# Performance work log

Hardware: AMD Instinct MI355X
Metric: run time of the kernel (lower is better)

## Reference

```python
import jax, jax.numpy as jnp
import numpy as np

N_HEADS = 6

def setup_inputs() -> dict:
    key = jax.random.key(0)
    k1, k2, k3 = jax.random.split(key, 3)
    B, T, C = 256, 256, 192
    x = jax.random.normal(k1, (B, T, C), dtype=jnp.float32)
    w_qkv = jax.random.normal(k2, (3 * C, C), dtype=jnp.float32) * (1.0 / np.sqrt(C))
    w_out = jax.random.normal(k3, (C, C), dtype=jnp.float32) * (1.0 / np.sqrt(C))
    return {"x": x, "w_qkv": w_qkv, "w_out": w_out}

def reference(x, w_qkv, w_out):
    B, T, C = x.shape
    H = N_HEADS
    D = C // H  # head_dim = 32
    qkv = (x @ w_qkv.T).reshape(B, T, 3, H, D)
    q, k, v = qkv[:, :, 0], qkv[:, :, 1], qkv[:, :, 2]  # [B,T,H,D]
    scale = 1.0 / jnp.sqrt(jnp.asarray(D, dtype=x.dtype))
    scores = jnp.einsum('bqhd,bkhd->bhqk', q, k) * scale  # [B,H,T,T]
    causal = jnp.tril(jnp.ones((T, T), dtype=bool))
    scores = jnp.where(causal[None, None], scores, jnp.finfo(x.dtype).min)
    attn = jax.nn.softmax(scores, axis=-1)
    y = jnp.einsum('bhqk,bkhd->bqhd', attn, v).reshape(B, T, C)
    return y @ w_out.T
```

## Files before the change

### kernel.cpp

```cpp
#include <hip/hip_runtime.h>


using f32x4  = __attribute__((ext_vector_type(4))) float;
using bf16x8 = __attribute__((ext_vector_type(8))) __bf16;
using u16x8  = __attribute__((ext_vector_type(8))) unsigned short;
using i32x4  = __attribute__((ext_vector_type(4))) int;

constexpr int Bn = 256;
constexpr int Tn = 256;
constexpr int Cn = 192;
constexpr int Hn = 6;
constexpr int Dn = 32;
constexpr int Mn = Bn * Tn;
constexpr float QSCALE = 0.2550533f;

__device__ __forceinline__ unsigned short f2bf(float f) {
  unsigned int u = __builtin_bit_cast(unsigned int, f);
  u += 0x7fffu + ((u >> 16) & 1u);
  return (unsigned short)(u >> 16);
}

__device__ __forceinline__ unsigned int cvtpk(float lo, float hi) {
  unsigned int r;
  asm("v_cvt_pk_bf16_f32 %0, %1, %2" : "=v"(r) : "v"(lo), "v"(hi));
  return r;
}

__device__ __forceinline__ f32x4 mfma16x16x32(u16x8 a, u16x8 b, f32x4 c) {
  return __builtin_amdgcn_mfma_f32_16x16x32_bf16(
      __builtin_bit_cast(bf16x8, a), __builtin_bit_cast(bf16x8, b), c, 0, 0, 0);
}

__global__ __launch_bounds__(256) void k_qkv(const float* __restrict__ x,
                                             const float* __restrict__ wqkv,
                                             unsigned short* __restrict__ qg,
                                             unsigned short* __restrict__ kg,
                                             unsigned short* __restrict__ vg) {
  __shared__ unsigned short As[64][200];
  __shared__ unsigned short Bs[64][200];
  const int m0 = blockIdx.x * 64;
  const int n0 = blockIdx.y * 64;
  const int tid = threadIdx.x;

#pragma unroll
  for (int it = 0; it < 12; ++it) {
    int f = tid + it * 256;
    int row = f / 48, c4 = (f % 48) * 4;
    float4 va = *reinterpret_cast<const float4*>(&x[(size_t)(m0 + row) * Cn + c4]);
    ushort4 ua; ua.x = f2bf(va.x); ua.y = f2bf(va.y); ua.z = f2bf(va.z); ua.w = f2bf(va.w);
    *reinterpret_cast<ushort4*>(&As[row][c4]) = ua;
    float4 vb = *reinterpret_cast<const float4*>(&wqkv[(size_t)(n0 + row) * Cn + c4]);
    ushort4 ub; ub.x = f2bf(vb.x); ub.y = f2bf(vb.y); ub.z = f2bf(vb.z); ub.w = f2bf(vb.w);
    *reinterpret_cast<ushort4*>(&Bs[row][c4]) = ub;
  }
  __syncthreads();

  const int wv = tid >> 6, lane = tid & 63, llo = lane & 15, lhi = lane >> 4;
  const int wm = (wv >> 1) * 32, wn = (wv & 1) * 32;
  f32x4 acc[2][2] = {};
#pragma unroll
  for (int ks = 0; ks < 6; ++ks) {
    u16x8 a[2], b[2];
#pragma unroll
    for (int i = 0; i < 2; ++i)
      a[i] = *reinterpret_cast<const u16x8*>(&As[wm + 16 * i + llo][ks * 32 + lhi * 8]);
#pragma unroll
    for (int j = 0; j < 2; ++j)
      b[j] = *reinterpret_cast<const u16x8*>(&Bs[wn + 16 * j + llo][ks * 32 + lhi * 8]);
#pragma unroll
    for (int i = 0; i < 2; ++i)
#pragma unroll
      for (int j = 0; j < 2; ++j)
        acc[i][j] = mfma16x16x32(a[i], b[j], acc[i][j]);
  }
#pragma unroll
  for (int i = 0; i < 2; ++i)
#pragma unroll
    for (int j = 0; j < 2; ++j)
#pragma unroll
      for (int r = 0; r < 4; ++r) {
        int mg = m0 + wm + 16 * i + lhi * 4 + r;
        int ng = n0 + wn + 16 * j + llo;
        int s = ng / 192;
        int rem = ng - s * 192;
        int h = rem >> 5, d = rem & 31;
        int bb = mg >> 8, t = mg & 255;
        float val = acc[i][j][r];
        unsigned short* dst = (s == 0) ? qg : (s == 1) ? kg : vg;
        float sv = (s == 0) ? val * QSCALE : val;
        dst[((size_t)(bb * Hn + h) * Tn + t) * Dn + d] = f2bf(sv);
      }
}

__global__ __launch_bounds__(256, 3) void k_attn(const unsigned short* __restrict__ qg,
                                                 const unsigned short* __restrict__ kg,
                                                 const unsigned short* __restrict__ vg,
                                                 unsigned short* __restrict__ yg) {
  __shared__ unsigned short Ks[256][40];
  __shared__ unsigned short Vt[32][264];
  const int bh = blockIdx.x;
  const int b = bh / Hn, h = bh - b * Hn;
  const size_t base = (size_t)bh * Tn * Dn;
  const int tid = threadIdx.x;

  {
    int row = tid;
    const unsigned short* kp = kg + base + (size_t)row * Dn;
    *reinterpret_cast<uint4*>(&Ks[row][0])  = *reinterpret_cast<const uint4*>(kp + 0);
    *reinterpret_cast<uint4*>(&Ks[row][8])  = *reinterpret_cast<const uint4*>(kp + 8);
    *reinterpret_cast<uint4*>(&Ks[row][16]) = *reinterpret_cast<const uint4*>(kp + 16);
    *reinterpret_cast<uint4*>(&Ks[row][24]) = *reinterpret_cast<const uint4*>(kp + 24);
    const unsigned short* vp = vg + base + (size_t)row * Dn;
    u16x8 v0 = *reinterpret_cast<const u16x8*>(vp + 0);
    u16x8 v1 = *reinterpret_cast<const u16x8*>(vp + 8);
    u16x8 v2 = *reinterpret_cast<const u16x8*>(vp + 16);
    u16x8 v3 = *reinterpret_cast<const u16x8*>(vp + 24);
#pragma unroll
    for (int e = 0; e < 8; ++e) {
      Vt[e][row]      = v0[e];
      Vt[8 + e][row]  = v1[e];
      Vt[16 + e][row] = v2[e];
      Vt[24 + e][row] = v3[e];
    }
  }
  __syncthreads();

  const int w = tid >> 6, lane = tid & 63, llo = lane & 15, lhi = lane >> 4;
  u16x8 qf[4];
  const unsigned short* qp = qg + base + (size_t)w * 64 * Dn;
#pragma unroll
  for (int i = 0; i < 4; ++i)
    qf[i] = *reinterpret_cast<const u16x8*>(qp + (size_t)(16 * i + llo) * Dn + lhi * 8);

  f32x4 ot[2][4] = {};
  float m_[4], l_[4];
#pragma unroll
  for (int qi = 0; qi < 4; ++qi) { m_[qi] = -1e30f; l_[qi] = 0.f; }

  const int addr0 = (llo + ((lhi & 1) << 5)) << 2;
  const int addr1 = addr0 + 64;

  for (int kt = 0; kt <= w; ++kt) {
    u16x8 kf[4];
#pragma unroll
    for (int kj = 0; kj < 4; ++kj)
      kf[kj] = *reinterpret_cast<const u16x8*>(&Ks[kt * 64 + kj * 16 + llo][lhi * 8]);
    u16x8 vtf[2][2];
#pragma unroll
    for (int ks = 0; ks < 2; ++ks)
#pragma unroll
      for (int dj = 0; dj < 2; ++dj)
        vtf[ks][dj] = *reinterpret_cast<const u16x8*>(&Vt[16 * dj + llo][kt * 64 + ks * 32 + lhi * 8]);

#pragma unroll
    for (int qi = 0; qi < 4; ++qi) {
      f32x4 st[4];
#pragma unroll
      for (int kj = 0; kj < 4; ++kj)
        st[kj] = mfma16x16x32(kf[kj], qf[qi], f32x4{});
      if (kt == w) {
        int ql = 16 * qi + llo;
#pragma unroll
        for (int kj = 0; kj < 4; ++kj)
#pragma unroll
          for (int r = 0; r < 4; ++r) {
            int kl = kj * 16 + lhi * 4 + r;
            st[kj][r] = (kl > ql) ? -1e30f : st[kj][r];
          }
      }
      float x0 = fmaxf(fmaxf(st[0][0], st[0][1]), fmaxf(st[0][2], st[0][3]));
      float x1 = fmaxf(fmaxf(st[1][0], st[1][1]), fmaxf(st[1][2], st[1][3]));
      float x2 = fmaxf(fmaxf(st[2][0], st[2][1]), fmaxf(st[2][2], st[2][3]));
      float x3 = fmaxf(fmaxf(st[3][0], st[3][1]), fmaxf(st[3][2], st[3][3]));
      float mx = fmaxf(fmaxf(x0, x1), fmaxf(x2, x3));
      mx = fmaxf(mx, __shfl_xor(mx, 16));
      mx = fmaxf(mx, __shfl_xor(mx, 32));
      float mn = fmaxf(m_[qi], mx);
      float al = exp2f(m_[qi] - mn);
      float sum = 0.f;
#pragma unroll
      for (int kj = 0; kj < 4; ++kj) {
        float p0 = exp2f(st[kj][0] - mn);
        float p1 = exp2f(st[kj][1] - mn);
        float p2 = exp2f(st[kj][2] - mn);
        float p3 = exp2f(st[kj][3] - mn);
        st[kj][0] = p0; st[kj][1] = p1; st[kj][2] = p2; st[kj][3] = p3;
        sum += (p0 + p1) + (p2 + p3);
      }
      sum += __shfl_xor(sum, 16);
      sum += __shfl_xor(sum, 32);
      l_[qi] = l_[qi] * al + sum;
      m_[qi] = mn;
#pragma unroll
      for (int dj = 0; dj < 2; ++dj)
#pragma unroll
        for (int r = 0; r < 4; ++r)
          ot[dj][qi][r] *= al;

      int pk0[4], pk1[4];
#pragma unroll
      for (int kj = 0; kj < 4; ++kj) {
        pk0[kj] = (int)cvtpk(st[kj][0], st[kj][1]);
        pk1[kj] = (int)cvtpk(st[kj][2], st[kj][3]);
      }
#pragma unroll
      for (int ks = 0; ks < 2; ++ks) {
        i32x4 pw;
#pragma unroll
        for (int j = 0; j < 4; ++j) {
          int addr = (j < 2) ? addr0 : addr1;
          int slo = (j & 1) ? pk1[2 * ks]     : pk0[2 * ks];
          int shi = (j & 1) ? pk1[2 * ks + 1] : pk0[2 * ks + 1];
          int blo = __builtin_amdgcn_ds_bpermute(addr, slo);
          int bhi = __builtin_amdgcn_ds_bpermute(addr, shi);
          pw[j] = (lhi & 2) ? bhi : blo;
        }
        u16x8 pbv = __builtin_bit_cast(u16x8, pw);
#pragma unroll
        for (int dj = 0; dj < 2; ++dj)
          ot[dj][qi] = mfma16x16x32(vtf[ks][dj], pbv, ot[dj][qi]);
      }
    }
  }
#pragma unroll
  for (int qi = 0; qi < 4; ++qi) {
    float rl = 1.0f / l_[qi];
    int t = w * 64 + 16 * qi + llo;
    size_t yo = ((size_t)(b * Tn + t) * Hn + h) * Dn;
#pragma unroll
    for (int dj = 0; dj < 2; ++dj) {
      uint2 pkd;
      pkd.x = cvtpk(ot[dj][qi][0] * rl, ot[dj][qi][1] * rl);
      pkd.y = cvtpk(ot[dj][qi][2] * rl, ot[dj][qi][3] * rl);
      *reinterpret_cast<uint2*>(&yg[yo + 16 * dj + lhi * 4]) = pkd;
    }
  }
}

__global__ __launch_bounds__(256) void k_out(const unsigned short* __restrict__ yg,
                                             const float* __restrict__ wout,
                                             float* __restrict__ out) {
  __shared__ unsigned short As[64][200];
  __shared__ unsigned short Bs[64][200];
  const int m0 = blockIdx.x * 64;
  const int n0 = blockIdx.y * 64;
  const int tid = threadIdx.x;

#pragma unroll
  for (int it = 0; it < 6; ++it) {
    int f = tid + it * 256;
    int row = f / 24, c8 = (f % 24) * 8;
    *reinterpret_cast<uint4*>(&As[row][c8]) =
        *reinterpret_cast<const uint4*>(&yg[(size_t)(m0 + row) * Cn + c8]);
  }
#pragma unroll
  for (int it = 0; it < 12; ++it) {
    int f = tid + it * 256;
    int row = f / 48, c4 = (f % 48) * 4;
    float4 vb = *reinterpret_cast<const float4*>(&wout[(size_t)(n0 + row) * Cn + c4]);
    ushort4 ub; ub.x = f2bf(vb.x); ub.y = f2bf(vb.y); ub.z = f2bf(vb.z); ub.w = f2bf(vb.w);
    *reinterpret_cast<ushort4*>(&Bs[row][c4]) = ub;
  }
  __syncthreads();

  const int wv = tid >> 6, lane = tid & 63, llo = lane & 15, lhi = lane >> 4;
  const int wm = (wv >> 1) * 32, wn = (wv & 1) * 32;
  f32x4 acc[2][2] = {};
#pragma unroll
  for (int ks = 0; ks < 6; ++ks) {
    u16x8 a[2], b[2];
#pragma unroll
    for (int i = 0; i < 2; ++i)
      a[i] = *reinterpret_cast<const u16x8*>(&As[wm + 16 * i + llo][ks * 32 + lhi * 8]);
#pragma unroll
    for (int j = 0; j < 2; ++j)
      b[j] = *reinterpret_cast<const u16x8*>(&Bs[wn + 16 * j + llo][ks * 32 + lhi * 8]);
#pragma unroll
    for (int i = 0; i < 2; ++i)
#pragma unroll
      for (int j = 0; j < 2; ++j)
        acc[i][j] = mfma16x16x32(a[i], b[j], acc[i][j]);
  }
#pragma unroll
  for (int i = 0; i < 2; ++i)
#pragma unroll
    for (int j = 0; j < 2; ++j)
#pragma unroll
      for (int r = 0; r < 4; ++r) {
        int mg = m0 + wm + 16 * i + lhi * 4 + r;
        int ng = n0 + wn + 16 * j + llo;
        out[(size_t)mg * Cn + ng] = acc[i][j][r];
      }
}

extern "C" void kernel_launch(void* const* d_in, const int* in_sizes, int n_in,
                              void* d_out, int out_size, void* d_ws, size_t ws_size,
                              hipStream_t stream) {
  const float* x    = (const float*)d_in[0];
  const float* wqkv = (const float*)d_in[1];
  const float* wout = (const float*)d_in[2];
  float* out = (float*)d_out;

  const size_t NE = (size_t)Mn * Cn;
  unsigned short* q = (unsigned short*)d_ws;
  unsigned short* k = q + NE;
  unsigned short* v = k + NE;
  unsigned short* y = v + NE;

  k_qkv<<<dim3(Mn / 64, (3 * Cn) / 64), 256, 0, stream>>>(x, wqkv, q, k, v);
  k_attn<<<dim3(Bn * Hn), 256, 0, stream>>>(q, k, v, y);
  k_out<<<dim3(Mn / 64, Cn / 64), 256, 0, stream>>>(y, wout, out);
}
```

Before: 131.7 us.

## Restructure projection GEMMs to keep activation rows in registers and loop over N

Both projection kernels now give each block 128 rows. Each wave holds its A fragments (x or y) in registers, loaded directly from global memory in MFMA fragment layout. The QKV kernel loops over all nine 64-column weight tiles with a double-buffered LDS tile, prefetching the next weight tile into registers while computing, and folds the Q scale into the weight conversion. The output kernel stages the whole of W_out in LDS once per block. This removes the repeated reads and bf16 conversions of x/y across the N-tile grid dimension, at the cost of fewer blocks, higher register pressure and redundant per-block weight conversion.

```diff
diff --git a/kernel.cpp b/kernel.cpp
--- a/kernel.cpp
+++ b/kernel.cpp
@@ -26,70 +26,112 @@
   return r;
 }
 
+__device__ __forceinline__ u16x8 pack8(float4 a, float4 b, float s) {
+  uint4 w;
+  w.x = cvtpk(a.x * s, a.y * s);
+  w.y = cvtpk(a.z * s, a.w * s);
+  w.z = cvtpk(b.x * s, b.y * s);
+  w.w = cvtpk(b.z * s, b.w * s);
+  return __builtin_bit_cast(u16x8, w);
+}
+
 __device__ __forceinline__ f32x4 mfma16x16x32(u16x8 a, u16x8 b, f32x4 c) {
   return __builtin_amdgcn_mfma_f32_16x16x32_bf16(
       __builtin_bit_cast(bf16x8, a), __builtin_bit_cast(bf16x8, b), c, 0, 0, 0);
 }
 
-__global__ __launch_bounds__(256) void k_qkv(const float* __restrict__ x,
-                                             const float* __restrict__ wqkv,
-                                             unsigned short* __restrict__ qg,
-                                             unsigned short* __restrict__ kg,
-                                             unsigned short* __restrict__ vg) {
-  __shared__ unsigned short As[64][200];
-  __shared__ unsigned short Bs[64][200];
-  const int m0 = blockIdx.x * 64;
-  const int n0 = blockIdx.y * 64;
+__global__ __launch_bounds__(256, 2) void k_qkv(const float* __restrict__ x,
+                                                const float* __restrict__ wqkv,
+                                                unsigned short* __restrict__ qg,
+                                                unsigned short* __restrict__ kg,
+                                                unsigned short* __restrict__ vg) {
+  __shared__ u16x8 Bsf[2][1536];
   const int tid = threadIdx.x;
-
-#pragma unroll
-  for (int it = 0; it < 12; ++it) {
-    int f = tid + it * 256;
-    int row = f / 48, c4 = (f % 48) * 4;
-    float4 va = *reinterpret_cast<const float4*>(&x[(size_t)(m0 + row) * Cn + c4]);
-    ushort4 ua; ua.x = f2bf(va.x); ua.y = f2bf(va.y); ua.z = f2bf(va.z); ua.w = f2bf(va.w);
-    *reinterpret_cast<ushort4*>(&As[row][c4]) = ua;
-    float4 vb = *reinterpret_cast<const float4*>(&wqkv[(size_t)(n0 + row) * Cn + c4]);
-    ushort4 ub; ub.x = f2bf(vb.x); ub.y = f2bf(vb.y); ub.z = f2bf(vb.z); ub.w = f2bf(vb.w);
-    *reinterpret_cast<ushort4*>(&Bs[row][c4]) = ub;
+  const int m0 = blockIdx.x * 128;
+  const int w = tid >> 6, lane = tid & 63, llo = lane & 15, lhi = lane >> 4;
+
+  u16x8 af[6][2];
+#pragma unroll
+  for (int i = 0; i < 2; ++i) {
+    const float* xr = x + (size_t)(m0 + 32 * w + 16 * i + llo) * Cn + lhi * 8;
+#pragma unroll
+    for (int ks = 0; ks < 6; ++ks) {
+      float4 a0 = *reinterpret_cast<const float4*>(xr + ks * 32);
+      float4 a1 = *reinterpret_cast<const float4*>(xr + ks * 32 + 4);
+      af[ks][i] = pack8(a0, a1, 1.0f);
+    }
+  }
+
+  {
+    const int n0 = 0;
+#pragma unroll
+    for (int it = 0; it < 6; ++it) {
+      int p = tid + it * 256;
+      int j = p / 384, rem = p - j * 384;
+      int ks = rem >> 6, l2 = rem & 63;
+      int row = j * 16 + (l2 & 15), col = ks * 32 + ((l2 >> 4) << 3);
+      const float* wp = wqkv + (size_t)(n0 + row) * Cn + col;
+      float4 a0 = *reinterpret_cast<const float4*>(wp);
+      float4 a1 = *reinterpret_cast<const float4*>(wp + 4);
+      Bsf[0][p] = pack8(a0, a1, QSCALE);
+    }
   }
   __syncthreads();
 
-  const int wv = tid >> 6, lane = tid & 63, llo = lane & 15, lhi = lane >> 4;
-  const int wm = (wv >> 1) * 32, wn = (wv & 1) * 32;
-  f32x4 acc[2][2] = {};
-#pragma unroll
-  for (int ks = 0; ks < 6; ++ks) {
-    u16x8 a[2], b[2];
+  for (int nt = 0; nt < 9; ++nt) {
+    const int cur = nt & 1;
+    float4 wr[6][2];
+    if (nt < 8) {
+      const int n0 = (nt + 1) * 64;
+#pragma unroll
+      for (int it = 0; it < 6; ++it) {
+        int p = tid + it * 256;
+        int j = p / 384, rem = p - j * 384;
+        int ks = rem >> 6, l2 = rem & 63;
+        int row = j * 16 + (l2 & 15), col = ks * 32 + ((l2 >> 4) << 3);
+        const float* wp = wqkv + (size_t)(n0 + row) * Cn + col;
+        wr[it][0] = *reinterpret_cast<const float4*>(wp);
+        wr[it][1] = *reinterpret_cast<const float4*>(wp + 4);
+      }
+    }
+    f32x4 acc[2][4] = {};
+#pragma unroll
+    for (int j = 0; j < 4; ++j) {
+      u16x8 bb[6];
+#pragma unroll
+      for (int ks = 0; ks < 6; ++ks)
+        bb[ks] = Bsf[cur][(j * 6 + ks) * 64 + lane];
+#pragma unroll
+      for (int ks = 0; ks < 6; ++ks)
+#pragma unroll
+        for (int i = 0; i < 2; ++i)
+          acc[i][j] = mfma16x16x32(af[ks][i], bb[ks], acc[i][j]);
+    }
+    if (nt < 8) {
+      const float sc = (nt + 1 < 3) ? QSCALE : 1.0f;
+#pragma unroll
+      for (int it = 0; it < 6; ++it) {
+        int p = tid + it * 256;
+        Bsf[cur ^ 1][p] = pack8(wr[it][0], wr[it][1], sc);
+      }
+    }
+    const int sidx = nt / 3;
+    unsigned short* dst = (sidx == 0) ? qg : (sidx == 1) ? kg : vg;
+    const int nbase = (nt - sidx * 3) * 64;
 #pragma unroll
     for (int i = 0; i < 2; ++i)
-      a[i] = *reinterpret_cast<const u16x8*>(&As[wm + 16 * i + llo][ks * 32 + lhi * 8]);
-#pragma unroll
-    for (int j = 0; j < 2; ++j)
-      b[j] = *reinterpret_cast<const u16x8*>(&Bs[wn + 16 * j + llo][ks * 32 + lhi * 8]);
-#pragma unroll
-    for (int i = 0; i < 2; ++i)
-#pragma unroll
-      for (int j = 0; j < 2; ++j)
-        acc[i][j] = mfma16x16x32(a[i], b[j], acc[i][j]);
-  }
-#pragma unroll
-  for (int i = 0; i < 2; ++i)
-#pragma unroll
-    for (int j = 0; j < 2; ++j)
-#pragma unroll
-      for (int r = 0; r < 4; ++r) {
-        int mg = m0 + wm + 16 * i + lhi * 4 + r;
-        int ng = n0 + wn + 16 * j + llo;
-        int s = ng / 192;
-        int rem = ng - s * 192;
-        int h = rem >> 5, d = rem & 31;
-        int bb = mg >> 8, t = mg & 255;
-        float val = acc[i][j][r];
-        unsigned short* dst = (s == 0) ? qg : (s == 1) ? kg : vg;
-        float sv = (s == 0) ? val * QSCALE : val;
-        dst[((size_t)(bb * Hn + h) * Tn + t) * Dn + d] = f2bf(sv);
-      }
+#pragma unroll
+      for (int j = 0; j < 4; ++j)
+#pragma unroll
+        for (int r = 0; r < 4; ++r) {
+          int mg = m0 + 32 * w + 16 * i + lhi * 4 + r;
+          int nn = nbase + 16 * j + llo;
+          int h = nn >> 5, d = nn & 31;
+          int bb_ = mg >> 8, t = mg & 255;
+          dst[(size_t)(bb_ * Hn + h) * (Tn * Dn) + t * Dn + d] = f2bf(acc[i][j][r]);
+        }
+    if (nt < 8) __syncthreads();
+  }
 }
 
 __global__ __launch_bounds__(256, 3) void k_attn(const unsigned short* __restrict__ qg,
@@ -237,58 +279,57 @@
   }
 }
 
-__global__ __launch_bounds__(256) void k_out(const unsigned short* __restrict__ yg,
-                                             const float* __restrict__ wout,
-                                             float* __restrict__ out) {
-  __shared__ unsigned short As[64][200];
-  __shared__ unsigned short Bs[64][200];
-  const int m0 = blockIdx.x * 64;
-  const int n0 = blockIdx.y * 64;
+__global__ __launch_bounds__(256, 2) void k_out(const unsigned short* __restrict__ yg,
+                                                const float* __restrict__ wout,
+                                                float* __restrict__ out) {
+  __shared__ u16x8 Bof[4608];
   const int tid = threadIdx.x;
-
-#pragma unroll
-  for (int it = 0; it < 6; ++it) {
-    int f = tid + it * 256;
-    int row = f / 24, c8 = (f % 24) * 8;
-    *reinterpret_cast<uint4*>(&As[row][c8]) =
-        *reinterpret_cast<const uint4*>(&yg[(size_t)(m0 + row) * Cn + c8]);
-  }
-#pragma unroll
-  for (int it = 0; it < 12; ++it) {
-    int f = tid + it * 256;
-    int row = f / 48, c4 = (f % 48) * 4;
-    float4 vb = *reinterpret_cast<const float4*>(&wout[(size_t)(n0 + row) * Cn + c4]);
-    ushort4 ub; ub.x = f2bf(vb.x); ub.y = f2bf(vb.y); ub.z = f2bf(vb.z); ub.w = f2bf(vb.w);
-    *reinterpret_cast<ushort4*>(&Bs[row][c4]) = ub;
+  const int m0 = blockIdx.x * 128;
+  const int w = tid >> 6, lane = tid & 63, llo = lane & 15, lhi = lane >> 4;
+
+#pragma unroll
+  for (int it = 0; it < 18; ++it) {
+    int p = tid + it * 256;
+    int j = p / 384, rem = p - j * 384;
+    int ks = rem >> 6, l2 = rem & 63;
+    int row = j * 16 + (l2 & 15), col = ks * 32 + ((l2 >> 4) << 3);
+    const float* wp = wout + (size_t)row * Cn + col;
+    float4 a0 = *reinterpret_cast<const float4*>(wp);
+    float4 a1 = *reinterpret_cast<const float4*>(wp + 4);
+    Bof[p] = pack8(a0, a1, 1.0f);
+  }
+
+  u16x8 af[6][2];
+#pragma unroll
+  for (int i = 0; i < 2; ++i) {
+    const unsigned short* yr = yg + (size_t)(m0 + 32 * w + 16 * i + llo) * Cn + lhi * 8;
+#pragma unroll
+    for (int ks = 0; ks < 6; ++ks)
+      af[ks][i] = *reinterpret_cast<const u16x8*>(yr + ks * 32);
   }
   __syncthreads();
 
-  const int wv = tid >> 6, lane = tid & 63, llo = lane & 15, lhi = lane >> 4;
-  const int wm = (wv >> 1) * 32, wn = (wv & 1) * 32;
-  f32x4 acc[2][2] = {};
-#pragma unroll
-  for (int ks = 0; ks < 6; ++ks) {
-    u16x8 a[2], b[2];
-#pragma unroll
-    for (int i = 0; i < 2; ++i)
-      a[i] = *reinterpret_cast<const u16x8*>(&As[wm + 16 * i + llo][ks * 32 + lhi * 8]);
-#pragma unroll
-    for (int j = 0; j < 2; ++j)
-      b[j] = *reinterpret_cast<const u16x8*>(&Bs[wn + 16 * j + llo][ks * 32 + lhi * 8]);
-#pragma unroll
-    for (int i = 0; i < 2; ++i)
-#pragma unroll
-      for (int j = 0; j < 2; ++j)
-        acc[i][j] = mfma16x16x32(a[i], b[j], acc[i][j]);
+  f32x4 acc[2][12] = {};
+#pragma unroll
+  for (int j = 0; j < 12; ++j) {
+    u16x8 bb[6];
+#pragma unroll
+    for (int ks = 0; ks < 6; ++ks)
+      bb[ks] = Bof[(j * 6 + ks) * 64 + lane];
+#pragma unroll
+    for (int ks = 0; ks < 6; ++ks)
+#pragma unroll
+      for (int i = 0; i < 2; ++i)
+        acc[i][j] = mfma16x16x32(af[ks][i], bb[ks], acc[i][j]);
   }
 #pragma unroll
   for (int i = 0; i < 2; ++i)
 #pragma unroll
-    for (int j = 0; j < 2; ++j)
+    for (int j = 0; j < 12; ++j)
 #pragma unroll
       for (int r = 0; r < 4; ++r) {
-        int mg = m0 + wm + 16 * i + lhi * 4 + r;
-        int ng = n0 + wn + 16 * j + llo;
+        int mg = m0 + 32 * w + 16 * i + lhi * 4 + r;
+        int ng = 16 * j + llo;
         out[(size_t)mg * Cn + ng] = acc[i][j][r];
       }
 }
@@ -307,7 +348,7 @@
   unsigned short* v = k + NE;
   unsigned short* y = v + NE;
 
-  k_qkv<<<dim3(Mn / 64, (3 * Cn) / 64), 256, 0, stream>>>(x, wqkv, q, k, v);
+  k_qkv<<<dim3(Mn / 128), 256, 0, stream>>>(x, wqkv, q, k, v);
   k_attn<<<dim3(Bn * Hn), 256, 0, stream>>>(q, k, v, y);
-  k_out<<<dim3(Mn / 64, Cn / 64), 256, 0, stream>>>(y, wout, out);
-}
+  k_out<<<dim3(Mn / 128), 256, 0, stream>>>(y, wout, out);
+}
```

Result: faster. 105.6 us (-19.8%).
